# Optimization experiments

Measured on AMD Instinct MI355X. Metric: run time of the kernel, lower is better.

The kernel has to match this reference:

```python
import jax, jax.numpy as jnp
import numpy as np

K_NN = 32
LN_EPS = 1e-5
P_JOINT = 0.95      # safety_priorities['structural_joints']
P_PLATFORM = 0.9    # safety_priorities['working_platforms']


def _sqdist(a, b):
    # a:[B,M,3], b:[B,N,3] -> [B,M,N] squared euclidean distances
    return jnp.maximum(jnp.sum(a * a, -1)[:, :, None] + jnp.sum(b * b, -1)[:, None, :]
                       - 2.0 * jnp.einsum('bmd,bnd->bmn', a, b), 0.0)


def _gather(arr, idx):
    # arr:[B,N,D], idx:[B,C] -> [B,C,D]
    B, C = idx.shape
    return jnp.take_along_axis(arr, jnp.broadcast_to(idx[:, :, None], (B, C, arr.shape[-1])), axis=1)


def _fps(coords, num_samples):
    # iterative farthest point sampling (deterministic start at index 0)
    B, N, _ = coords.shape
    start = jnp.zeros((B,), jnp.int32)
    dist0 = jnp.full((B, N), jnp.inf, coords.dtype)
    samp0 = jnp.zeros((B, num_samples), jnp.int32)

    def body(i, carry):
        dist, samp, last = carry
        last_pts = _gather(coords, last[:, None])                 # [B,1,3]
        d = jnp.sqrt(jnp.sum((coords - last_pts) ** 2, -1))       # [B,N]
        dist = jnp.minimum(dist, d)
        nxt = jnp.argmax(dist, 1).astype(jnp.int32)
        dist = dist.at[jnp.arange(B), nxt].set(0.0)
        samp = samp.at[:, i].set(nxt)
        return dist, samp, nxt

    _, samp, _ = jax.lax.fori_loop(1, num_samples, body, (dist0, samp0, start))
    return samp


def _safety(coords, scale):
    # per-point safety score [B,N], computed on the full point cloud (as in original)
    N = coords.shape[1]
    z = coords[:, :, 2]
    if scale == 'global':
        return 1.0 + jax.nn.sigmoid((z - z.mean(1, keepdims=True)) / 5.0) * P_JOINT
    if scale == 'component':
        zv = jnp.var(z, axis=1, keepdims=True, ddof=1)            # torch.var is unbiased
        return jnp.broadcast_to(1.0 + jnp.exp(-zv / 0.1) * P_PLATFORM, z.shape)
    # detail: full NxN cdist -> connection density (dist < 0.5  <=>  sqdist < 0.25)
    d2 = _sqdist(coords, coords)                                  # [B,N,N]
    density = jnp.sum(d2 < 0.25, -1).astype(coords.dtype)
    return 1.0 + density / N * P_JOINT


def _select_scale(features, coords, C, S, W1, b1, W2, b2, scale):
    idx = _fps(coords, C)                     # [B,C]
    cfeat = _gather(features, idx)            # [B,C,D]
    ccoord = _gather(coords, idx)             # [B,C,3]
    # kNN max-pooled local features (computed by original module; not used downstream)
    knn_d2 = _sqdist(ccoord, coords)          # [B,C,N]
    _, knn = jax.lax.top_k(-knn_d2, K_NN)
    _local = jax.vmap(lambda f, i: f[i])(features, knn).max(2)    # [B,C,D]
    # per-center safety score: per-point score gathered at FPS centers
    safety = jnp.take_along_axis(_safety(coords, scale), idx, axis=1)  # [B,C]
    # selector MLP: Linear -> ReLU -> Linear -> Sigmoid
    probs = jax.nn.sigmoid(jnp.maximum(cfeat @ W1.T + b1, 0.0) @ W2.T + b2)  # [B,C,S]
    final = probs.mean(-1) * safety           # [B,C] per-center score
    _, top = jax.lax.top_k(final, S)          # [B,S]
    return _gather(cfeat, top)                # [B,S,D]


def _forward(pf, pc, g_W1, g_b1, g_W2, g_b2, c_W1, c_b1, c_W2, c_b2,
             d_W1, d_b1, d_W2, d_b2, p_W1, p_b1, p_W2, p_b2, ln_g, ln_b):
    g = _select_scale(pf, pc, 256, 16, g_W1, g_b1, g_W2, g_b2, 'global')
    c = _select_scale(pf, pc, 128, 16, c_W1, c_b1, c_W2, c_b2, 'component')
    d = _select_scale(pf, pc, 64, 8, d_W1, d_b1, d_W2, d_b2, 'detail')
    toks = jnp.concatenate([g, c, d], 1)      # [B,40,D]
    # prompt_mlp: Linear(D,D/2) -> ReLU -> Linear(D/2,D) -> LayerNorm(D)
    h = jnp.maximum(toks @ p_W1.T + p_b1, 0.0) @ p_W2.T + p_b2
    mu = h.mean(-1, keepdims=True)
    var = h.var(-1, keepdims=True)
    return (h - mu) * jax.lax.rsqrt(var + LN_EPS) * ln_g + ln_b


def setup_inputs() -> dict:
    key = jax.random.key(0)
    B, N, D = 2, 8192, 768
    ks = iter(jax.random.split(key, 32))

    def nrm(shape, s=0.02):
        return jax.random.normal(next(ks), shape, jnp.float32) * s

    inp = {
        'point_features': jax.random.normal(next(ks), (B, N, D), jnp.float32),
        'point_coords': jax.random.normal(next(ks), (B, N, 3), jnp.float32) * 2.0,
    }
    for p, C, S in [('g', 256, 16), ('c', 128, 16), ('d', 64, 8)]:
        inp[p + '_W1'] = nrm((C, D)); inp[p + '_b1'] = jnp.zeros((C,), jnp.float32)
        inp[p + '_W2'] = nrm((S, C)); inp[p + '_b2'] = jnp.zeros((S,), jnp.float32)
    inp['p_W1'] = nrm((D // 2, D)); inp['p_b1'] = jnp.zeros((D // 2,), jnp.float32)
    inp['p_W2'] = nrm((D, D // 2)); inp['p_b2'] = jnp.zeros((D,), jnp.float32)
    inp['ln_g'] = jnp.ones((D,), jnp.float32); inp['ln_b'] = jnp.zeros((D,), jnp.float32)
    return inp


def reference(point_features, point_coords, g_W1, g_b1, g_W2, g_b2,
              c_W1, c_b1, c_W2, c_b2, d_W1, d_b1, d_W2, d_b2,
              p_W1, p_b1, p_W2, p_b2, ln_g, ln_b):
    return _forward(point_features, point_coords, g_W1, g_b1, g_W2, g_b2,
                    c_W1, c_b1, c_W2, c_b2, d_W1, d_b1, d_W2, d_b2,
                    p_W1, p_b1, p_W2, p_b2, ln_g, ln_b)
```

## Files before the change

kernel.cpp:

```cpp
#include <hip/hip_runtime.h>
#include <math.h>

#define N_PTS 8192
#define D_FEAT 768

__device__ __forceinline__ float wred_max_f32(float x) {
    int v = __float_as_int(x), o;
    o = __builtin_amdgcn_update_dpp(0, v, 0x111, 0xf, 0xf, false); v = __float_as_int(fmaxf(__int_as_float(v), __int_as_float(o)));
    o = __builtin_amdgcn_update_dpp(0, v, 0x112, 0xf, 0xf, false); v = __float_as_int(fmaxf(__int_as_float(v), __int_as_float(o)));
    o = __builtin_amdgcn_update_dpp(0, v, 0x114, 0xf, 0xf, false); v = __float_as_int(fmaxf(__int_as_float(v), __int_as_float(o)));
    o = __builtin_amdgcn_update_dpp(0, v, 0x118, 0xf, 0xf, false); v = __float_as_int(fmaxf(__int_as_float(v), __int_as_float(o)));
    o = __builtin_amdgcn_update_dpp(0, v, 0x142, 0xa, 0xf, false); v = __float_as_int(fmaxf(__int_as_float(v), __int_as_float(o)));
    o = __builtin_amdgcn_update_dpp(0, v, 0x143, 0xc, 0xf, false); v = __float_as_int(fmaxf(__int_as_float(v), __int_as_float(o)));
    return __int_as_float(__builtin_amdgcn_readlane(v, 63));
}
__device__ __forceinline__ int wred_min_i32(int x) {
    int v = x, o;
    o = __builtin_amdgcn_update_dpp(0x7fffffff, v, 0x111, 0xf, 0xf, false); v = (o < v) ? o : v;
    o = __builtin_amdgcn_update_dpp(0x7fffffff, v, 0x112, 0xf, 0xf, false); v = (o < v) ? o : v;
    o = __builtin_amdgcn_update_dpp(0x7fffffff, v, 0x114, 0xf, 0xf, false); v = (o < v) ? o : v;
    o = __builtin_amdgcn_update_dpp(0x7fffffff, v, 0x118, 0xf, 0xf, false); v = (o < v) ? o : v;
    o = __builtin_amdgcn_update_dpp(0x7fffffff, v, 0x142, 0xa, 0xf, false); v = (o < v) ? o : v;
    o = __builtin_amdgcn_update_dpp(0x7fffffff, v, 0x143, 0xc, 0xf, false); v = (o < v) ? o : v;
    return __builtin_amdgcn_readlane(v, 63);
}
__device__ __forceinline__ float wred_add_f32(float x) {
    int v = __float_as_int(x), o;
    o = __builtin_amdgcn_update_dpp(0, v, 0x111, 0xf, 0xf, false); v = __float_as_int(__int_as_float(v) + __int_as_float(o));
    o = __builtin_amdgcn_update_dpp(0, v, 0x112, 0xf, 0xf, false); v = __float_as_int(__int_as_float(v) + __int_as_float(o));
    o = __builtin_amdgcn_update_dpp(0, v, 0x114, 0xf, 0xf, false); v = __float_as_int(__int_as_float(v) + __int_as_float(o));
    o = __builtin_amdgcn_update_dpp(0, v, 0x118, 0xf, 0xf, false); v = __float_as_int(__int_as_float(v) + __int_as_float(o));
    o = __builtin_amdgcn_update_dpp(0, v, 0x142, 0xa, 0xf, false); v = __float_as_int(__int_as_float(v) + __int_as_float(o));
    o = __builtin_amdgcn_update_dpp(0, v, 0x143, 0xc, 0xf, false); v = __float_as_int(__int_as_float(v) + __int_as_float(o));
    return __int_as_float(__builtin_amdgcn_readlane(v, 63));
}

#define DPP64_STEP(cur, ctrl, rmask)                                                        \
    {                                                                                       \
        unsigned _h = (unsigned)__builtin_amdgcn_update_dpp(0, (int)(unsigned)((cur) >> 32), ctrl, rmask, 0xf, false); \
        unsigned _l = (unsigned)__builtin_amdgcn_update_dpp(0, (int)(unsigned)(cur), ctrl, rmask, 0xf, false);         \
        unsigned long long _o = ((unsigned long long)_h << 32) | _l;                        \
        cur = (_o > (cur)) ? _o : (cur);                                                    \
    }

__global__ __launch_bounds__(256, 1) __attribute__((amdgpu_waves_per_eu(1)))
void fps_kernel(const float* __restrict__ coords,
                int* __restrict__ idx_all,
                float* __restrict__ safety_all) {
#pragma clang fp contract(off)
    const int b = blockIdx.x;
    const int t = threadIdx.x;
    const float* cb = coords + (size_t)b * N_PTS * 3;

    float px[32], py[32], pz[32], m2[32];
#pragma unroll
    for (int k = 0; k < 32; k++) {
        int p = t + k * 256;
        px[k] = cb[p * 3 + 0];
        py[k] = cb[p * 3 + 1];
        pz[k] = cb[p * 3 + 2];
        m2[k] = INFINITY;
    }
    __shared__ unsigned long long skey[2][4];
    __shared__ int sel[256];
    __shared__ float r1s[4], r2s[4];
    if (t == 0) sel[0] = 0;
    float lx = cb[0], ly = cb[1], lz = cb[2];
    __syncthreads();

    const int lane = t & 63, w = t >> 6;
    for (int i = 1; i < 256; i++) {
#pragma unroll
        for (int k = 0; k < 32; k++) {
            float dx = px[k] - lx, dy = py[k] - ly, dz = pz[k] - lz;
            float d2 = dx * dx + dy * dy + dz * dz;
            m2[k] = fminf(m2[k], d2);
        }
        float t0[16];
#pragma unroll
        for (int k = 0; k < 16; k++) t0[k] = fmaxf(m2[k], m2[k + 16]);
#pragma unroll
        for (int k = 0; k < 8; k++) t0[k] = fmaxf(t0[k], t0[k + 8]);
#pragma unroll
        for (int k = 0; k < 4; k++) t0[k] = fmaxf(t0[k], t0[k + 4]);
        float c2 = fmaxf(fmaxf(t0[0], t0[1]), fmaxf(t0[2], t0[3]));
        int ci[16];
#pragma unroll
        for (int k = 0; k < 16; k++) {
            int a  = (m2[k]      == c2) ? k        : 0x7fff;
            int bb = (m2[k + 16] == c2) ? (k + 16) : 0x7fff;
            ci[k] = (a < bb) ? a : bb;
        }
#pragma unroll
        for (int k = 0; k < 8; k++) ci[k] = min(ci[k], ci[k + 8]);
#pragma unroll
        for (int k = 0; k < 4; k++) ci[k] = min(ci[k], ci[k + 4]);
        int bk = min(min(ci[0], ci[1]), min(ci[2], ci[3]));
        float thi = c2 * 0.9999995f;
        int ncnt = 0;
#pragma unroll
        for (int k = 0; k < 32; k++) ncnt += (m2[k] >= thi) ? 1 : 0;
        float smax;
        if (__any(ncnt >= 2)) {
            float sd[32];
#pragma unroll
            for (int k = 0; k < 32; k++) sd[k] = sqrtf(m2[k]);
            smax = sd[0]; bk = 0;
#pragma unroll
            for (int k = 1; k < 32; k++) if (sd[k] > smax) { smax = sd[k]; bk = k; }
        } else {
            smax = sqrtf(c2);
        }
        int bi = t + bk * 256;
        unsigned long long key = ((unsigned long long)__float_as_uint(smax) << 32)
                               | (unsigned)(0xFFFFFFFFu - (unsigned)bi);
        DPP64_STEP(key, 0x111, 0xf)
        DPP64_STEP(key, 0x112, 0xf)
        DPP64_STEP(key, 0x114, 0xf)
        DPP64_STEP(key, 0x118, 0xf)
        DPP64_STEP(key, 0x142, 0xa)
        DPP64_STEP(key, 0x143, 0xc)
        if (lane == 63) skey[i & 1][w] = key;
        __syncthreads();
        const int par = i & 1;
        unsigned long long k8 = skey[par][lane & 3];
        int cidx = (int)(0xFFFFFFFFu - (unsigned)k8);
        float spec = 0.f;
        if (lane < 12) spec = cb[cidx * 3 + (lane >> 2)];
        DPP64_STEP(k8, 0x111, 0xf)
        DPP64_STEP(k8, 0x112, 0xf)
        unsigned klo = (unsigned)__builtin_amdgcn_readlane((int)(unsigned)k8, 3);
        int fbi = (int)(0xFFFFFFFFu - klo);
        int ww = (fbi & 255) >> 6;
        lx = __int_as_float(__builtin_amdgcn_readlane(__float_as_int(spec), ww));
        ly = __int_as_float(__builtin_amdgcn_readlane(__float_as_int(spec), 4 + ww));
        lz = __int_as_float(__builtin_amdgcn_readlane(__float_as_int(spec), 8 + ww));
        if (t == 0) sel[i] = fbi;
    }

    __syncthreads();
    {
        int v = sel[t];
        idx_all[b * 256 + t] = v;
        if (t < 128) idx_all[512 + b * 128 + t] = v;
        if (t < 64)  idx_all[768 + b * 64 + t] = v;
    }

    float s1 = 0.f, s2 = 0.f;
#pragma unroll
    for (int k = 0; k < 32; k++) { s1 += pz[k]; s2 += pz[k] * pz[k]; }
    s1 = wred_add_f32(s1);
    s2 = wred_add_f32(s2);
    if (lane == 0) { r1s[w] = s1; r2s[w] = s2; }
    __syncthreads();
    float S1 = r1s[0] + r1s[1] + r1s[2] + r1s[3];
    float S2 = r2s[0] + r2s[1] + r2s[2] + r2s[3];
    float mean = S1 / 8192.0f;
    float var1 = (S2 - S1 * S1 / 8192.0f) / 8191.0f;
    float scomp = 1.0f + expf(-var1 / 0.1f) * 0.9f;
    {
        int p = sel[t];
        float z = cb[p * 3 + 2];
        safety_all[b * 256 + t] = 1.0f + (1.0f / (1.0f + expf(-((z - mean) / 5.0f)))) * 0.95f;
    }
    if (t < 128) safety_all[512 + b * 128 + t] = scomp;
}

__global__ __launch_bounds__(256) void score_kernel(
    const float* __restrict__ feat, const float* __restrict__ coords,
    const float* __restrict__ gW1, const float* __restrict__ gb1,
    const float* __restrict__ gW2, const float* __restrict__ gb2,
    const float* __restrict__ cW1, const float* __restrict__ cb1,
    const float* __restrict__ cW2, const float* __restrict__ cb2,
    const float* __restrict__ dW1, const float* __restrict__ db1,
    const float* __restrict__ dW2, const float* __restrict__ db2,
    const int* __restrict__ idx_all, const float* __restrict__ safety_all,
    float* __restrict__ final_all) {
    int bid = blockIdx.x;
    int b, c0, C, S, off;
    const float *W1, *b1, *W2, *b2;
    if (bid < 64)      { C = 256; S = 16; W1 = gW1; b1 = gb1; W2 = gW2; b2 = gb2; b = bid >> 5; c0 = (bid & 31) * 8; off = 0; }
    else if (bid < 96) { int r = bid - 64; C = 128; S = 16; W1 = cW1; b1 = cb1; W2 = cW2; b2 = cb2; b = r >> 4; c0 = (r & 15) * 8; off = 512; }
    else               { int r = bid - 96; C = 64;  S = 8;  W1 = dW1; b1 = db1; W2 = dW2; b2 = db2; b = r >> 3; c0 = (r & 7) * 8; off = 768; }
    const bool isdet = (bid >= 96);

    __shared__ float xt[8 * 772];
    __shared__ float h1s[8 * 260];
    __shared__ float ps[8 * 16];
    __shared__ int pid[8];
    __shared__ float dpart[4][8];
    __shared__ float sdens[8];
    const int t = threadIdx.x;
    if (t < 8) pid[t] = idx_all[off + b * C + c0 + t];
    __syncthreads();

    if (isdet) {
#pragma clang fp contract(off)
        float cx[8], cy[8], cz[8], cc[8];
#pragma unroll
        for (int c = 0; c < 8; c++) {
            const float* cp = coords + ((size_t)b * N_PTS + pid[c]) * 3;
            cx[c] = cp[0]; cy[c] = cp[1]; cz[c] = cp[2];
            cc[c] = cx[c] * cx[c] + cy[c] * cy[c] + cz[c] * cz[c];
        }
        int cnt[8];
#pragma unroll
        for (int c = 0; c < 8; c++) cnt[c] = 0;
        const float* cbl = coords + (size_t)b * N_PTS * 3;
        for (int k = 0; k < 32; k++) {
            int q = t + k * 256;
            float x = cbl[q * 3], y = cbl[q * 3 + 1], z = cbl[q * 3 + 2];
            float pp = x * x + y * y + z * z;
#pragma unroll
            for (int c = 0; c < 8; c++) {
                float dot = cx[c] * x + cy[c] * y + cz[c] * z;
                float d2 = (cc[c] + pp) - 2.0f * dot;
                if (d2 < 0.25f) cnt[c]++;
            }
        }
        int wv = t >> 6;
#pragma unroll
        for (int c = 0; c < 8; c++) {
            float s = wred_add_f32((float)cnt[c]);
            if ((t & 63) == 0) dpart[wv][c] = s;
        }
    }

    for (int r = 0; r < 8; r++) {
        const float* src = feat + ((size_t)b * N_PTS + pid[r]) * D_FEAT;
        for (int c = t; c < 768; c += 256) xt[r * 772 + c] = src[c];
    }
    __syncthreads();
    if (isdet && t < 8) {
        float tot = dpart[0][t] + dpart[1][t] + dpart[2][t] + dpart[3][t];
        sdens[t] = 1.0f + (tot / 8192.0f) * 0.95f;
    }

    {
        int rp = t & 3;
        int jg = t >> 2;
        int r0 = rp * 2;
        if (jg * 4 < C) {
            float4 acc0[4], acc1[4];
#pragma unroll
            for (int a = 0; a < 4; a++) { acc0[a] = make_float4(0, 0, 0, 0); acc1[a] = make_float4(0, 0, 0, 0); }
            for (int k = 0; k < 768; k += 4) {
                float4 x0 = *(const float4*)&xt[r0 * 772 + k];
                float4 x1 = *(const float4*)&xt[(r0 + 1) * 772 + k];
#pragma unroll
                for (int a = 0; a < 4; a++) {
                    int j = jg * 4 + a;
                    float4 wv = *(const float4*)&W1[(size_t)j * 768 + k];
                    acc0[a].x = fmaf(wv.x, x0.x, acc0[a].x); acc0[a].y = fmaf(wv.y, x0.y, acc0[a].y);
                    acc0[a].z = fmaf(wv.z, x0.z, acc0[a].z); acc0[a].w = fmaf(wv.w, x0.w, acc0[a].w);
                    acc1[a].x = fmaf(wv.x, x1.x, acc1[a].x); acc1[a].y = fmaf(wv.y, x1.y, acc1[a].y);
                    acc1[a].z = fmaf(wv.z, x1.z, acc1[a].z); acc1[a].w = fmaf(wv.w, x1.w, acc1[a].w);
                }
            }
#pragma unroll
            for (int a = 0; a < 4; a++) {
                int j = jg * 4 + a;
                float bb = b1[j];
                float v0 = (acc0[a].x + acc0[a].y) + (acc0[a].z + acc0[a].w) + bb;
                float v1 = (acc1[a].x + acc1[a].y) + (acc1[a].z + acc1[a].w) + bb;
                h1s[r0 * 260 + j]       = fmaxf(v0, 0.f);
                h1s[(r0 + 1) * 260 + j] = fmaxf(v1, 0.f);
            }
        }
    }
    __syncthreads();

    if (t < 8 * S) {
        int r = t / S, s = t % S;
        float4 a = make_float4(0, 0, 0, 0);
        for (int k = 0; k < C; k += 4) {
            float4 wv = *(const float4*)&W2[s * C + k];
            float4 h = *(const float4*)&h1s[r * 260 + k];
            a.x = fmaf(wv.x, h.x, a.x); a.y = fmaf(wv.y, h.y, a.y);
            a.z = fmaf(wv.z, h.z, a.z); a.w = fmaf(wv.w, h.w, a.w);
        }
        float logit = (a.x + a.y) + (a.z + a.w) + b2[s];
        ps[r * 16 + s] = 1.0f / (1.0f + expf(-logit));
    }
    __syncthreads();
    if (t < 8) {
        float m = 0.f;
        for (int s = 0; s < S; s++) m += ps[t * 16 + s];
        m /= (float)S;
        float saf = isdet ? sdens[t] : safety_all[off + b * C + c0 + t];
        final_all[off + b * C + c0 + t] = m * saf;
    }
}

__global__ __launch_bounds__(256) void final_kernel(
    const float* __restrict__ feat, const int* __restrict__ idx_all,
    const float* __restrict__ final_all,
    const float* __restrict__ pW1, const float* __restrict__ pb1,
    const float* __restrict__ pW2, const float* __restrict__ pb2,
    const float* __restrict__ lng, const float* __restrict__ lnb,
    float* __restrict__ out) {
    int bid = blockIdx.x;
    int b = bid / 20, pr = bid % 20;
    int t = threadIdx.x;
    __shared__ float xt[2 * 772];
    __shared__ float h1s[2 * 388];
    __shared__ float red[16];
    __shared__ int tokp[2];

    int scale = (pr < 8) ? 0 : (pr < 16) ? 1 : 2;
    int C    = (scale == 0) ? 256 : (scale == 1) ? 128 : 64;
    int off  = (scale == 0) ? 0 : (scale == 1) ? 512 : 768;
    int base = (scale == 0) ? 0 : (scale == 1) ? 8 : 16;
    int r0 = (pr - base) * 2;

    if (t < 64) {
        float v[4];
#pragma unroll
        for (int j = 0; j < 4; j++) {
            int ii = t + j * 64;
            v[j] = (ii < C) ? final_all[off + b * C + ii] : -INFINITY;
        }
        for (int s = 0; s <= r0 + 1; s++) {
            float bd = v[0]; int bj = 0;
#pragma unroll
            for (int j = 1; j < 4; j++) if (v[j] > bd) { bd = v[j]; bj = j; }
            int bi2 = t + bj * 64;
            float m = wred_max_f32(bd);
            int cand = (bd == m) ? bi2 : 0x7fffffff;
            int wi = wred_min_i32(cand);
            if (t == (wi & 63)) {
#pragma unroll
                for (int j = 0; j < 4; j++) if (j == (wi >> 6)) v[j] = -INFINITY;
            }
            if (t == 0) {
                if (s == r0)     tokp[0] = idx_all[off + b * C + wi];
                if (s == r0 + 1) tokp[1] = idx_all[off + b * C + wi];
            }
        }
    }
    __syncthreads();

    for (int r = 0; r < 2; r++) {
        int p = tokp[r];
        const float* src = feat + ((size_t)b * N_PTS + p) * D_FEAT;
        for (int c = t; c < 768; c += 256) xt[r * 772 + c] = src[c];
    }
    __syncthreads();

    for (int u = t; u < 768; u += 256) {
        int j = u >> 1, r = u & 1;
        float4 a = make_float4(0, 0, 0, 0);
        for (int k = 0; k < 768; k += 4) {
            float4 wv = *(const float4*)&pW1[(size_t)j * 768 + k];
            float4 x = *(const float4*)&xt[r * 772 + k];
            a.x = fmaf(wv.x, x.x, a.x); a.y = fmaf(wv.y, x.y, a.y);
            a.z = fmaf(wv.z, x.z, a.z); a.w = fmaf(wv.w, x.w, a.w);
        }
        float v = (a.x + a.y) + (a.z + a.w) + pb1[j];
        h1s[r * 388 + j] = fmaxf(v, 0.f);
    }
    __syncthreads();

    for (int u = t; u < 1536; u += 256) {
        int o = u >> 1, r = u & 1;
        float4 a = make_float4(0, 0, 0, 0);
        for (int k = 0; k < 384; k += 4) {
            float4 wv = *(const float4*)&pW2[(size_t)o * 384 + k];
            float4 h = *(const float4*)&h1s[r * 388 + k];
            a.x = fmaf(wv.x, h.x, a.x); a.y = fmaf(wv.y, h.y, a.y);
            a.z = fmaf(wv.z, h.z, a.z); a.w = fmaf(wv.w, h.w, a.w);
        }
        xt[r * 772 + o] = (a.x + a.y) + (a.z + a.w) + pb2[o];
    }
    __syncthreads();

    for (int r = 0; r < 2; r++) {
        float s1 = 0.f, s2 = 0.f;
        for (int o = t; o < 768; o += 256) { float v = xt[r * 772 + o]; s1 += v; s2 += v * v; }
#pragma unroll
        for (int off2 = 32; off2 >= 1; off2 >>= 1) {
            s1 += __shfl_down(s1, off2, 64);
            s2 += __shfl_down(s2, off2, 64);
        }
        int lane = t & 63, wid = t >> 6;
        if (lane == 0) { red[wid * 2] = s1; red[wid * 2 + 1] = s2; }
        __syncthreads();
        float S1 = red[0] + red[2] + red[4] + red[6];
        float S2 = red[1] + red[3] + red[5] + red[7];
        float mu = S1 / 768.0f;
        float var = S2 / 768.0f - mu * mu;
        float inv = rsqrtf(var + 1e-5f);
        float* dst = out + ((size_t)b * 40 + pr * 2 + r) * 768;
        for (int o = t; o < 768; o += 256) {
            float v = xt[r * 772 + o];
            dst[o] = (v - mu) * inv * lng[o] + lnb[o];
        }
        __syncthreads();
    }
}

extern "C" void kernel_launch(void* const* d_in, const int* in_sizes, int n_in,
                              void* d_out, int out_size, void* d_ws, size_t ws_size,
                              hipStream_t stream) {
    const float* feat   = (const float*)d_in[0];
    const float* coords = (const float*)d_in[1];
    const float* gW1 = (const float*)d_in[2],  *gb1 = (const float*)d_in[3];
    const float* gW2 = (const float*)d_in[4],  *gb2 = (const float*)d_in[5];
    const float* cW1 = (const float*)d_in[6],  *cb1 = (const float*)d_in[7];
    const float* cW2 = (const float*)d_in[8],  *cb2 = (const float*)d_in[9];
    const float* dW1 = (const float*)d_in[10], *db1 = (const float*)d_in[11];
    const float* dW2 = (const float*)d_in[12], *db2 = (const float*)d_in[13];
    const float* pW1 = (const float*)d_in[14], *pb1 = (const float*)d_in[15];
    const float* pW2 = (const float*)d_in[16], *pb2 = (const float*)d_in[17];
    const float* lng = (const float*)d_in[18], *lnb = (const float*)d_in[19];
    float* out = (float*)d_out;

    int*   idx_all    = (int*)d_ws;
    float* safety_all = (float*)d_ws + 896;
    float* final_all  = (float*)d_ws + 1792;

    fps_kernel<<<2, 256, 0, stream>>>(coords, idx_all, safety_all);
    score_kernel<<<112, 256, 0, stream>>>(feat, coords, gW1, gb1, gW2, gb2, cW1, cb1, cW2, cb2,
                                          dW1, db1, dW2, db2, idx_all, safety_all, final_all);
    final_kernel<<<40, 256, 0, stream>>>(feat, idx_all, final_all, pW1, pb1, pW2, pb2, lng, lnb, out);
}
```

Before: 617.9 us.

## Pack FPS distance math into float2 vectors and cache coords in LDS

Rewrites the farthest-point-sampling inner loop to use 2-wide float vectors so the compiler can emit packed FP32 ops (v_pk_*), halving the instruction count for the distance and min/max reductions. The argmax-index search becomes a single reverse select chain. The near-tie detection becomes a wave-wide ballot popcount. Coordinates are also staged in a 128KB LDS array so the per-iteration fetch of the selected point reads LDS instead of global memory, which adds shared memory use and may change tie-handling semantics slightly.

```diff
diff --git a/kernel.cpp b/kernel.cpp
--- a/kernel.cpp
+++ b/kernel.cpp
@@ -3,6 +3,8 @@
 
 #define N_PTS 8192
 #define D_FEAT 768
+
+typedef float v2f __attribute__((ext_vector_type(2)));
 
 __device__ __forceinline__ float wred_max_f32(float x) {
     int v = __float_as_int(x), o;
@@ -52,62 +54,69 @@
     const int t = threadIdx.x;
     const float* cb = coords + (size_t)b * N_PTS * 3;
 
-    float px[32], py[32], pz[32], m2[32];
-#pragma unroll
-    for (int k = 0; k < 32; k++) {
-        int p = t + k * 256;
-        px[k] = cb[p * 3 + 0];
-        py[k] = cb[p * 3 + 1];
-        pz[k] = cb[p * 3 + 2];
-        m2[k] = INFINITY;
-    }
+    v2f px2[16], py2[16], pz2[16], m2p[16];
+#pragma unroll
+    for (int j = 0; j < 16; j++) {
+        int p0 = t + (2 * j) * 256, p1 = t + (2 * j + 1) * 256;
+        px2[j].x = cb[p0 * 3 + 0]; px2[j].y = cb[p1 * 3 + 0];
+        py2[j].x = cb[p0 * 3 + 1]; py2[j].y = cb[p1 * 3 + 1];
+        pz2[j].x = cb[p0 * 3 + 2]; pz2[j].y = cb[p1 * 3 + 2];
+        m2p[j].x = INFINITY; m2p[j].y = INFINITY;
+    }
+    __shared__ float cbl4[N_PTS * 4];
     __shared__ unsigned long long skey[2][4];
     __shared__ int sel[256];
     __shared__ float r1s[4], r2s[4];
+#pragma unroll
+    for (int j = 0; j < 16; j++) {
+        int p0 = t + (2 * j) * 256, p1 = t + (2 * j + 1) * 256;
+        *(float4*)&cbl4[p0 * 4] = make_float4(px2[j].x, py2[j].x, pz2[j].x, 0.f);
+        *(float4*)&cbl4[p1 * 4] = make_float4(px2[j].y, py2[j].y, pz2[j].y, 0.f);
+    }
     if (t == 0) sel[0] = 0;
     float lx = cb[0], ly = cb[1], lz = cb[2];
     __syncthreads();
 
     const int lane = t & 63, w = t >> 6;
     for (int i = 1; i < 256; i++) {
-#pragma unroll
-        for (int k = 0; k < 32; k++) {
-            float dx = px[k] - lx, dy = py[k] - ly, dz = pz[k] - lz;
-            float d2 = dx * dx + dy * dy + dz * dz;
-            m2[k] = fminf(m2[k], d2);
-        }
-        float t0[16];
-#pragma unroll
-        for (int k = 0; k < 16; k++) t0[k] = fmaxf(m2[k], m2[k + 16]);
-#pragma unroll
-        for (int k = 0; k < 8; k++) t0[k] = fmaxf(t0[k], t0[k + 8]);
-#pragma unroll
-        for (int k = 0; k < 4; k++) t0[k] = fmaxf(t0[k], t0[k + 4]);
-        float c2 = fmaxf(fmaxf(t0[0], t0[1]), fmaxf(t0[2], t0[3]));
-        int ci[16];
-#pragma unroll
-        for (int k = 0; k < 16; k++) {
-            int a  = (m2[k]      == c2) ? k        : 0x7fff;
-            int bb = (m2[k + 16] == c2) ? (k + 16) : 0x7fff;
-            ci[k] = (a < bb) ? a : bb;
-        }
-#pragma unroll
-        for (int k = 0; k < 8; k++) ci[k] = min(ci[k], ci[k + 8]);
-#pragma unroll
-        for (int k = 0; k < 4; k++) ci[k] = min(ci[k], ci[k + 4]);
-        int bk = min(min(ci[0], ci[1]), min(ci[2], ci[3]));
+        v2f Lx = {lx, lx}, Ly = {ly, ly}, Lz = {lz, lz};
+#pragma unroll
+        for (int j = 0; j < 16; j++) {
+            v2f dx = px2[j] - Lx, dy = py2[j] - Ly, dz = pz2[j] - Lz;
+            v2f d2 = dx * dx + dy * dy + dz * dz;
+            m2p[j] = __builtin_elementwise_min(m2p[j], d2);
+        }
+        v2f q[8];
+#pragma unroll
+        for (int j = 0; j < 8; j++) q[j] = __builtin_elementwise_max(m2p[j], m2p[j + 8]);
+#pragma unroll
+        for (int j = 0; j < 4; j++) q[j] = __builtin_elementwise_max(q[j], q[j + 4]);
+        q[0] = __builtin_elementwise_max(q[0], q[2]);
+        q[1] = __builtin_elementwise_max(q[1], q[3]);
+        q[0] = __builtin_elementwise_max(q[0], q[1]);
+        float c2 = fmaxf(q[0].x, q[0].y);
+        int bk = 0;
+#pragma unroll
+        for (int j = 15; j >= 0; j--) {
+            bk = (m2p[j].y == c2) ? (2 * j + 1) : bk;
+            bk = (m2p[j].x == c2) ? (2 * j) : bk;
+        }
         float thi = c2 * 0.9999995f;
-        int ncnt = 0;
-#pragma unroll
-        for (int k = 0; k < 32; k++) ncnt += (m2[k] >= thi) ? 1 : 0;
+        int tot = 0;
+#pragma unroll
+        for (int j = 0; j < 16; j++) {
+            tot += __popcll(__ballot(m2p[j].x >= thi));
+            tot += __popcll(__ballot(m2p[j].y >= thi));
+        }
         float smax;
-        if (__any(ncnt >= 2)) {
-            float sd[32];
-#pragma unroll
-            for (int k = 0; k < 32; k++) sd[k] = sqrtf(m2[k]);
-            smax = sd[0]; bk = 0;
-#pragma unroll
-            for (int k = 1; k < 32; k++) if (sd[k] > smax) { smax = sd[k]; bk = k; }
+        if (tot > 64) {
+            smax = -1.f; bk = 0;
+#pragma unroll
+            for (int k = 0; k < 32; k++) {
+                float mk = (k & 1) ? m2p[k >> 1].y : m2p[k >> 1].x;
+                float s = sqrtf(mk);
+                if (s > smax) { smax = s; bk = k; }
+            }
         } else {
             smax = sqrtf(c2);
         }
@@ -126,7 +135,7 @@
         unsigned long long k8 = skey[par][lane & 3];
         int cidx = (int)(0xFFFFFFFFu - (unsigned)k8);
         float spec = 0.f;
-        if (lane < 12) spec = cb[cidx * 3 + (lane >> 2)];
+        if (lane < 12) spec = cbl4[cidx * 4 + (lane >> 2)];
         DPP64_STEP(k8, 0x111, 0xf)
         DPP64_STEP(k8, 0x112, 0xf)
         unsigned klo = (unsigned)__builtin_amdgcn_readlane((int)(unsigned)k8, 3);
@@ -148,7 +157,10 @@
 
     float s1 = 0.f, s2 = 0.f;
 #pragma unroll
-    for (int k = 0; k < 32; k++) { s1 += pz[k]; s2 += pz[k] * pz[k]; }
+    for (int j = 0; j < 16; j++) {
+        s1 += pz2[j].x; s2 += pz2[j].x * pz2[j].x;
+        s1 += pz2[j].y; s2 += pz2[j].y * pz2[j].y;
+    }
     s1 = wred_add_f32(s1);
     s2 = wred_add_f32(s2);
     if (lane == 0) { r1s[w] = s1; r2s[w] = s2; }
@@ -160,7 +172,7 @@
     float scomp = 1.0f + expf(-var1 / 0.1f) * 0.9f;
     {
         int p = sel[t];
-        float z = cb[p * 3 + 2];
+        float z = cbl4[p * 4 + 2];
         safety_all[b * 256 + t] = 1.0f + (1.0f / (1.0f + expf(-((z - mean) / 5.0f)))) * 0.95f;
     }
     if (t < 128) safety_all[512 + b * 128 + t] = scomp;
```

Result: slower. 639.6 us (+3.5%).
